# Kernel optimization log

Hardware: AMD Instinct MI355X
Metric: run time of the kernel (lower is better)

Reference implementation:

```python
import jax, jax.numpy as jnp
import numpy as np
from jax import lax

R = 3
D = (2 * R + 1) ** 2  # 49 local offsets


def _unfold(x, r):
    # torch F.unfold(kernel=2r+1, padding=r): (B,C,H,W) -> (B, C*K*K, H, W),
    # channel-major (c, ky, kx) ordering, matching conv_general_dilated_patches.
    k = 2 * r + 1
    return lax.conv_general_dilated_patches(
        x, (k, k), (1, 1), [(r, r), (r, r)],
        dimension_numbers=("NCHW", "OIHW", "NCHW"))


def _l2norm(x, eps=1e-12):
    n = jnp.sqrt(jnp.sum(x * x, axis=1, keepdims=True))
    return x / jnp.maximum(n, eps)


def setup_inputs() -> dict:
    key = jax.random.key(0)
    ks = jax.random.split(key, 8)
    B, Cin, Cmid, H, W = 2, 256, 128, 112, 112
    phi_cur = jax.random.normal(ks[0], (B, Cin, H, W), jnp.float32)
    phi_rnd = jax.random.normal(ks[1], (B, Cin, H, W), jnp.float32)
    P_cur = jax.random.normal(ks[2], (B, 3, H, W), jnp.float32)
    P_rnd = jax.random.normal(ks[3], (B, 3, H, W), jnp.float32)
    Wq = jax.random.normal(ks[4], (Cmid, Cin), jnp.float32) * 0.05
    Wk = jax.random.normal(ks[5], (Cmid, Cin), jnp.float32) * 0.05
    Wv = jax.random.normal(ks[6], (D, D), jnp.float32) * 0.1
    bv = jnp.zeros((D,), jnp.float32)
    gamma = jnp.array(1.0, jnp.float32)
    return dict(phi_cur=phi_cur, phi_rnd=phi_rnd, P_cur=P_cur, P_rnd=P_rnd,
                Wq=Wq, Wk=Wk, Wv=Wv, bv=bv, gamma=gamma)


def reference(phi_cur, phi_rnd, P_cur, P_rnd, Wq, Wk, Wv, bv, gamma):
    B, _, H, W = phi_cur.shape
    # 1x1 convs + channel L2 normalize
    q = _l2norm(jnp.einsum('oc,bchw->bohw', Wq, phi_cur))
    k = _l2norm(jnp.einsum('oc,bchw->bohw', Wk, phi_rnd))
    # local cost volume: patches (B, Cmid, D, H, W)
    patches = _unfold(k, R).reshape(B, -1, D, H, W)
    corr = jnp.einsum('bchw,bcdhw->bdhw', q, patches)  # (B,D,H,W)
    vol_corr = jnp.einsum('ed,bdhw->behw', Wv, corr) + bv[None, :, None, None]
    # geometric bias
    Pr = _unfold(P_rnd, R).reshape(B, 3, D, H, W)
    dP = P_cur[:, :, None, :, :] - Pr  # (B,3,D,H,W)
    dz = dP[:, 2]
    dist = jnp.sqrt(jnp.clip(jnp.sum(dP * dP, axis=1), 1e-12, None))
    logits = vol_corr + gamma * (-dist - 0.5 * jnp.abs(dz))
    w = jax.nn.softmax(logits, axis=1)
    off = jnp.arange(-R, R + 1, dtype=w.dtype)
    dY, dX = jnp.meshgrid(off, off, indexing='ij')
    offx = dX.reshape(1, D, 1, 1)
    offy = dY.reshape(1, D, 1, 1)
    du = jnp.sum(w * offx, axis=1, keepdims=True)
    dv = jnp.sum(w * offy, axis=1, keepdims=True)
    conf = jnp.max(w, axis=1, keepdims=True)
    return du, dv, conf
```

## Files before the change

### kernel.cpp

```cpp
#include <hip/hip_runtime.h>
#include <hip/hip_bf16.h>
#include <math.h>

constexpr int B    = 2;
constexpr int CIN  = 256;
constexpr int CMID = 128;
constexpr int H    = 112;
constexpr int W    = 112;
constexpr int HW   = H * W;
constexpr int NPIX = B * HW;
constexpr int RAD  = 3;
constexpr int KS   = 7;
constexpr int DD   = 49;

typedef __attribute__((ext_vector_type(8))) short  short8;
typedef __attribute__((ext_vector_type(4))) float  float4v;

__device__ __forceinline__ unsigned pkbf(float a, float b) {
    __hip_bfloat162 h = __float22bfloat162_rn(make_float2(a, b));
    union { __hip_bfloat162 h2; unsigned u; } c;
    c.h2 = h;
    return c.u;
}

constexpr int PSTR = 264;

__global__ __launch_bounds__(256) void proj_mfma(
    const float* __restrict__ phi_cur, const float* __restrict__ phi_rnd,
    const float* __restrict__ Wq, const float* __restrict__ Wk,
    unsigned short* __restrict__ q_ws, unsigned short* __restrict__ k_ws)
{
    __shared__ unsigned short pt[64 * PSTR];
    __shared__ float red[4][64];

    const int tid  = threadIdx.x;
    const int lane = tid & 63;
    const int wv   = __builtin_amdgcn_readfirstlane(tid >> 6);
    const int t    = blockIdx.y;

    const float* __restrict__ phi  = t ? phi_rnd : phi_cur;
    const float* __restrict__ Wf   = t ? Wk : Wq;
    unsigned short* __restrict__ outp = t ? k_ws : q_ws;

    const int pgb = blockIdx.x * 64;
    const int b   = pgb / HW;
    const int pim = pgb % HW;
    const float* pbase = phi + (size_t)b * CIN * HW + pim;

#pragma unroll
    for (int pass = 0; pass < 8; ++pass) {
        const int idx = pass * 256 + tid;
        const int cp  = idx >> 4;
        const int pq  = idx & 15;
        const int c0  = cp * 2;
        const float4 va = *(const float4*)(pbase + (size_t)c0 * HW + pq * 4);
        const float4 vb = *(const float4*)(pbase + (size_t)(c0 + 1) * HW + pq * 4);
        *(unsigned*)(pt + (pq * 4 + 0) * PSTR + c0) = pkbf(va.x, vb.x);
        *(unsigned*)(pt + (pq * 4 + 1) * PSTR + c0) = pkbf(va.y, vb.y);
        *(unsigned*)(pt + (pq * 4 + 2) * PSTR + c0) = pkbf(va.z, vb.z);
        *(unsigned*)(pt + (pq * 4 + 3) * PSTR + c0) = pkbf(va.w, vb.w);
    }

    const int m = lane & 15, quad = lane >> 4;
    short8 af[2][8];
#pragma unroll
    for (int ot = 0; ot < 2; ++ot)
#pragma unroll
        for (int kc = 0; kc < 8; ++kc) {
            const float* wr = Wf + (size_t)(wv * 32 + ot * 16 + m) * CIN
                                 + kc * 32 + quad * 8;
            const float4 w0 = *(const float4*)(wr);
            const float4 w1 = *(const float4*)(wr + 4);
            union { short8 s; unsigned u[4]; } cv;
            cv.u[0] = pkbf(w0.x, w0.y);
            cv.u[1] = pkbf(w0.z, w0.w);
            cv.u[2] = pkbf(w1.x, w1.y);
            cv.u[3] = pkbf(w1.z, w1.w);
            af[ot][kc] = cv.s;
        }

    __syncthreads();

    float4v acc[2][4];
#pragma unroll
    for (int ot = 0; ot < 2; ++ot)
#pragma unroll
        for (int nt = 0; nt < 4; ++nt) acc[ot][nt] = (float4v)0.f;

#pragma unroll
    for (int kc = 0; kc < 8; ++kc) {
        short8 bf[4];
#pragma unroll
        for (int nt = 0; nt < 4; ++nt)
            bf[nt] = *(const short8*)(pt + (nt * 16 + m) * PSTR + kc * 32 + quad * 8);
#pragma unroll
        for (int ot = 0; ot < 2; ++ot)
#pragma unroll
            for (int nt = 0; nt < 4; ++nt)
                acc[ot][nt] = __builtin_amdgcn_mfma_f32_16x16x32_bf16(
                    af[ot][kc], bf[nt], acc[ot][nt], 0, 0, 0);
    }

#pragma unroll
    for (int nt = 0; nt < 4; ++nt) {
        float ss = 0.f;
#pragma unroll
        for (int ot = 0; ot < 2; ++ot)
#pragma unroll
            for (int r = 0; r < 4; ++r)
                ss = fmaf(acc[ot][nt][r], acc[ot][nt][r], ss);
        ss += __shfl_xor(ss, 16, 64);
        ss += __shfl_xor(ss, 32, 64);
        if (quad == 0) red[wv][nt * 16 + m] = ss;
    }
    __syncthreads();

    float inv[4];
#pragma unroll
    for (int nt = 0; nt < 4; ++nt) {
        const int px = nt * 16 + m;
        const float tot = red[0][px] + red[1][px] + red[2][px] + red[3][px];
        inv[nt] = 1.f / fmaxf(sqrtf(tot), 1e-12f);
    }

#pragma unroll
    for (int nt = 0; nt < 4; ++nt)
#pragma unroll
        for (int ot = 0; ot < 2; ++ot) {
            uint2 st;
            st.x = pkbf(acc[ot][nt][0] * inv[nt], acc[ot][nt][1] * inv[nt]);
            st.y = pkbf(acc[ot][nt][2] * inv[nt], acc[ot][nt][3] * inv[nt]);
            *(uint2*)(outp + (size_t)(pgb + nt * 16 + m) * CMID
                      + wv * 32 + ot * 16 + quad * 4) = st;
        }
}

constexpr int TILE = 16;
constexpr int COLS = TILE + 6;
constexpr int NV   = KS * COLS;
constexpr int KSTR = 136;

__global__ __launch_bounds__(256) void corr_kernel(
    const unsigned short* __restrict__ q_ws, const unsigned short* __restrict__ k_ws,
    const float* __restrict__ P_cur, const float* __restrict__ P_rnd,
    const float* __restrict__ Wvm, const float* __restrict__ bv,
    const float* __restrict__ gamma_p, float* __restrict__ out)
{
    __shared__ unsigned short kt[NV * KSTR];
    __shared__ alignas(16) unsigned short qt[TILE * KSTR];
    __shared__ float cs[TILE][52];

    const int tid  = threadIdx.x;
    const int lane = tid & 63;
    const int wv   = __builtin_amdgcn_readfirstlane(tid >> 6);
    const int w0   = blockIdx.x * TILE;
    const int h    = blockIdx.y;
    const int b    = blockIdx.z;

    const int sub  = tid & 15;
    const int vgrp = tid >> 4;
#pragma unroll
    for (int pass = 0; pass < 10; ++pass) {
        const int vi = pass * 16 + vgrp;
        if (vi < NV) {
            const int rr = vi / COLS;
            const int cc = vi % COLS;
            const int hh = h + rr - RAD;
            const int ww = w0 + cc - RAD;
            uint4 v = make_uint4(0, 0, 0, 0);
            if (hh >= 0 && hh < H && ww >= 0 && ww < W)
                v = *(const uint4*)(k_ws + (size_t)(b * HW + hh * W + ww) * CMID + sub * 8);
            *(uint4*)(kt + vi * KSTR + sub * 8) = v;
        }
    }
    {
        const uint4 v = *(const uint4*)(q_ws + (size_t)(b * HW + h * W + w0 + vgrp) * CMID + sub * 8);
        *(uint4*)(qt + vgrp * KSTR + sub * 8) = v;
    }

    const int  ld    = (lane < DD) ? lane : 0;
    const bool valid = (lane < DD);
    float wrow[52];
#pragma unroll
    for (int e = 0; e < DD; ++e) wrow[e] = Wvm[ld * DD + e];
    wrow[49] = wrow[50] = wrow[51] = 0.f;
    const float bvv   = bv[ld];
    const float gamma = gamma_p[0];

    __syncthreads();

    if (tid < TILE * 3)
        cs[tid / 3][49 + tid % 3] = 0.f;

    const int m = lane & 15, quad = lane >> 4;
    for (int g = wv; g < 14; g += 4) {
        const int r  = g >> 1;
        const int nt = g & 1;
        const int vi = min(r * COLS + nt * 16 + m, NV - 1);
        float4v acc = (float4v)0.f;
#pragma unroll
        for (int kc = 0; kc < 4; ++kc) {
            const short8 afrag = *(const short8*)(qt + m * KSTR + kc * 32 + quad * 8);
            const short8 bfrag = *(const short8*)(kt + vi * KSTR + kc * 32 + quad * 8);
            acc = __builtin_amdgcn_mfma_f32_16x16x32_bf16(afrag, bfrag, acc, 0, 0, 0);
        }
#pragma unroll
        for (int reg = 0; reg < 4; ++reg) {
            const int p   = quad * 4 + reg;
            const int off = nt * 16 + m - p;
            if (off >= 0 && off <= 6)
                cs[p][r * 7 + off] = acc[reg];
        }
    }
    __syncthreads();
    float* lsf = reinterpret_cast<float*>(qt);

    const int dy = ld / KS - RAD;
    const int dx = ld % KS - RAD;

#pragma unroll
    for (int i = 0; i < 4; ++i) {
        const int pl = wv * 4 + i;

        const int hn = h + dy, wn = w0 + pl + dx;
        const bool inb = valid && hn >= 0 && hn < H && wn >= 0 && wn < W;
        const float* pc = P_cur + (size_t)b * 3 * HW + (h * W + w0 + pl);
        const float cx = pc[0], cy = pc[HW], cz = pc[2 * HW];
        float rx = 0.f, ry = 0.f, rz = 0.f;
        if (inb) {
            const float* pr = P_rnd + (size_t)b * 3 * HW + (hn * W + wn);
            rx = pr[0]; ry = pr[HW]; rz = pr[2 * HW];
        }
        const float dpx = cx - rx, dpy = cy - ry, dpz = cz - rz;
        const float dist = sqrtf(fmaxf(dpx * dpx + dpy * dpy + dpz * dpz, 1e-12f));

        float logit = -INFINITY;
        if (valid) {
            float v = bvv;
#pragma unroll
            for (int e4 = 0; e4 < 13; ++e4) {
                const float4 c4 = *(const float4*)&cs[pl][e4 * 4];
                v = fmaf(wrow[e4 * 4 + 0], c4.x, v);
                v = fmaf(wrow[e4 * 4 + 1], c4.y, v);
                v = fmaf(wrow[e4 * 4 + 2], c4.z, v);
                v = fmaf(wrow[e4 * 4 + 3], c4.w, v);
            }
            logit = v + gamma * (-dist - 0.5f * fabsf(dpz));
        }
        lsf[pl * 64 + lane] = logit;
    }

    {
        const int pli = lane >> 4;
        const int dq  = lane & 15;
        const int pl  = wv * 4 + pli;

        const float4 v = ((const float4*)lsf)[pl * 16 + dq];

        float m4 = fmaxf(fmaxf(v.x, v.y), fmaxf(v.z, v.w));
#pragma unroll
        for (int s = 1; s < 16; s <<= 1)
            m4 = fmaxf(m4, __shfl_xor(m4, s, 64));

        const float e0 = __expf(v.x - m4);
        const float e1 = __expf(v.y - m4);
        const float e2 = __expf(v.z - m4);
        const float e3 = __expf(v.w - m4);
        float Z = (e0 + e1) + (e2 + e3);

        const int c0i = dq * 4;
        float dus = 0.f, dvs = 0.f;
        {
            const float ex[4] = { e0, e1, e2, e3 };
#pragma unroll
            for (int j = 0; j < 4; ++j) {
                const int col = c0i + j;
                dus = fmaf(ex[j], (float)(col % KS - RAD), dus);
                dvs = fmaf(ex[j], (float)(col / KS - RAD), dvs);
            }
        }
#pragma unroll
        for (int s = 1; s < 16; s <<= 1) {
            Z   += __shfl_xor(Z,   s, 64);
            dus += __shfl_xor(dus, s, 64);
            dvs += __shfl_xor(dvs, s, 64);
        }

        if (dq == 0) {
            const int pg = b * HW + h * W + w0 + pl;
            const float invZ = 1.f / Z;
            out[pg]            = dus * invZ;
            out[NPIX + pg]     = dvs * invZ;
            out[2 * NPIX + pg] = invZ;
        }
    }
}

extern "C" void kernel_launch(void* const* d_in, const int* in_sizes, int n_in,
                              void* d_out, int out_size, void* d_ws, size_t ws_size,
                              hipStream_t stream)
{
    const float* phi_cur = (const float*)d_in[0];
    const float* phi_rnd = (const float*)d_in[1];
    const float* P_cur   = (const float*)d_in[2];
    const float* P_rnd   = (const float*)d_in[3];
    const float* Wq      = (const float*)d_in[4];
    const float* Wk      = (const float*)d_in[5];
    const float* Wv      = (const float*)d_in[6];
    const float* bv      = (const float*)d_in[7];
    const float* gm      = (const float*)d_in[8];
    float* out = (float*)d_out;

    unsigned short* ws   = (unsigned short*)d_ws;
    unsigned short* q_ws = ws;
    unsigned short* k_ws = q_ws + (size_t)NPIX * CMID;

    proj_mfma<<<dim3(NPIX / 64, 2), 256, 0, stream>>>(
        phi_cur, phi_rnd, Wq, Wk, q_ws, k_ws);

    corr_kernel<<<dim3(W / TILE, H, B), 256, 0, stream>>>(
        q_ws, k_ws, P_cur, P_rnd, Wv, bv, gm, out);
}
```

Baseline: 141.5 us.

## Pre-convert weights to bf16, swizzle LDS, remap corr blocks, split FMA chains

A new prep kernel converts Wq/Wk to bf16 once and pads Wv rows to 52 floats. The projection kernel then streams A fragments straight from the bf16 weights inside the k-loop instead of holding 16 short8 registers per thread. It also XOR-swizzles the LDS layout of the phi tile to cut bank conflicts, and its launch bounds now ask for 4 blocks per CU. The corr kernel remaps block IDs so neighbouring blocks are spread across XCDs, loads Wv as float4, and splits the 49-term dot product into two accumulators for more ILP. In exchange it adds an extra kernel launch and re-reads weights from global/L2 on every k step.

```diff
diff --git a/kernel.cpp b/kernel.cpp
--- a/kernel.cpp
+++ b/kernel.cpp
@@ -23,11 +23,34 @@
     return c.u;
 }
 
+__global__ __launch_bounds__(256) void prep(
+    const float* __restrict__ Wq, const float* __restrict__ Wk,
+    const float* __restrict__ Wv,
+    unsigned short* __restrict__ wqb, unsigned short* __restrict__ wkb,
+    float* __restrict__ wvp)
+{
+    if (blockIdx.x < 64) {
+        const int i  = blockIdx.x * 256 + threadIdx.x;
+        const int n4 = (CMID * CIN) / 4;
+        const float4 v = (i < n4) ? ((const float4*)Wq)[i] : ((const float4*)Wk)[i - n4];
+        uint2 r;
+        r.x = pkbf(v.x, v.y);
+        r.y = pkbf(v.z, v.w);
+        if (i < n4) ((uint2*)wqb)[i] = r;
+        else        ((uint2*)wkb)[i - n4] = r;
+    } else {
+        for (int idx = threadIdx.x; idx < DD * 52; idx += 256) {
+            const int r = idx / 52, c = idx % 52;
+            wvp[idx] = (c < DD) ? Wv[r * DD + c] : 0.f;
+        }
+    }
+}
+
 constexpr int PSTR = 264;
 
-__global__ __launch_bounds__(256) void proj_mfma(
+__global__ __launch_bounds__(256, 4) void proj_mfma(
     const float* __restrict__ phi_cur, const float* __restrict__ phi_rnd,
-    const float* __restrict__ Wq, const float* __restrict__ Wk,
+    const unsigned short* __restrict__ wq_bf, const unsigned short* __restrict__ wk_bf,
     unsigned short* __restrict__ q_ws, unsigned short* __restrict__ k_ws)
 {
     __shared__ unsigned short pt[64 * PSTR];
@@ -38,9 +61,9 @@
     const int wv   = __builtin_amdgcn_readfirstlane(tid >> 6);
     const int t    = blockIdx.y;
 
-    const float* __restrict__ phi  = t ? phi_rnd : phi_cur;
-    const float* __restrict__ Wf   = t ? Wk : Wq;
-    unsigned short* __restrict__ outp = t ? k_ws : q_ws;
+    const float* __restrict__ phi          = t ? phi_rnd : phi_cur;
+    const unsigned short* __restrict__ Wbf = t ? wk_bf : wq_bf;
+    unsigned short* __restrict__ outp      = t ? k_ws : q_ws;
 
     const int pgb = blockIdx.x * 64;
     const int b   = pgb / HW;
@@ -53,52 +76,43 @@
         const int cp  = idx >> 4;
         const int pq  = idx & 15;
         const int c0  = cp * 2;
+        const int swz = ((pq >> 1) & 3) << 3;
         const float4 va = *(const float4*)(pbase + (size_t)c0 * HW + pq * 4);
         const float4 vb = *(const float4*)(pbase + (size_t)(c0 + 1) * HW + pq * 4);
-        *(unsigned*)(pt + (pq * 4 + 0) * PSTR + c0) = pkbf(va.x, vb.x);
-        *(unsigned*)(pt + (pq * 4 + 1) * PSTR + c0) = pkbf(va.y, vb.y);
-        *(unsigned*)(pt + (pq * 4 + 2) * PSTR + c0) = pkbf(va.z, vb.z);
-        *(unsigned*)(pt + (pq * 4 + 3) * PSTR + c0) = pkbf(va.w, vb.w);
-    }
+        const int col = c0 ^ swz;
+        *(unsigned*)(pt + (pq * 4 + 0) * PSTR + col) = pkbf(va.x, vb.x);
+        *(unsigned*)(pt + (pq * 4 + 1) * PSTR + col) = pkbf(va.y, vb.y);
+        *(unsigned*)(pt + (pq * 4 + 2) * PSTR + col) = pkbf(va.z, vb.z);
+        *(unsigned*)(pt + (pq * 4 + 3) * PSTR + col) = pkbf(va.w, vb.w);
+    }
+
+    __syncthreads();
 
     const int m = lane & 15, quad = lane >> 4;
-    short8 af[2][8];
+    float4v acc[2][4];
 #pragma unroll
     for (int ot = 0; ot < 2; ++ot)
 #pragma unroll
-        for (int kc = 0; kc < 8; ++kc) {
-            const float* wr = Wf + (size_t)(wv * 32 + ot * 16 + m) * CIN
-                                 + kc * 32 + quad * 8;
-            const float4 w0 = *(const float4*)(wr);
-            const float4 w1 = *(const float4*)(wr + 4);
-            union { short8 s; unsigned u[4]; } cv;
-            cv.u[0] = pkbf(w0.x, w0.y);
-            cv.u[1] = pkbf(w0.z, w0.w);
-            cv.u[2] = pkbf(w1.x, w1.y);
-            cv.u[3] = pkbf(w1.z, w1.w);
-            af[ot][kc] = cv.s;
-        }
-
-    __syncthreads();
-
-    float4v acc[2][4];
-#pragma unroll
-    for (int ot = 0; ot < 2; ++ot)
-#pragma unroll
         for (int nt = 0; nt < 4; ++nt) acc[ot][nt] = (float4v)0.f;
 
 #pragma unroll
     for (int kc = 0; kc < 8; ++kc) {
-        short8 bf[4];
-#pragma unroll
-        for (int nt = 0; nt < 4; ++nt)
-            bf[nt] = *(const short8*)(pt + (nt * 16 + m) * PSTR + kc * 32 + quad * 8);
-#pragma unroll
-        for (int ot = 0; ot < 2; ++ot)
-#pragma unroll
-            for (int nt = 0; nt < 4; ++nt)
-                acc[ot][nt] = __builtin_amdgcn_mfma_f32_16x16x32_bf16(
-                    af[ot][kc], bf[nt], acc[ot][nt], 0, 0, 0);
+        const short8 af0 = *(const short8*)(Wbf +
+            (size_t)(wv * 32 + m) * CIN + kc * 32 + quad * 8);
+        const short8 af1 = *(const short8*)(Wbf +
+            (size_t)(wv * 32 + 16 + m) * CIN + kc * 32 + quad * 8);
+        short8 bfr[4];
+#pragma unroll
+        for (int nt = 0; nt < 4; ++nt) {
+            const int row = nt * 16 + m;
+            const int col = (kc * 32 + quad * 8) ^ (((row >> 3) & 3) << 3);
+            bfr[nt] = *(const short8*)(pt + row * PSTR + col);
+        }
+#pragma unroll
+        for (int nt = 0; nt < 4; ++nt) {
+            acc[0][nt] = __builtin_amdgcn_mfma_f32_16x16x32_bf16(af0, bfr[nt], acc[0][nt], 0, 0, 0);
+            acc[1][nt] = __builtin_amdgcn_mfma_f32_16x16x32_bf16(af1, bfr[nt], acc[1][nt], 0, 0, 0);
+        }
     }
 
 #pragma unroll
@@ -143,7 +157,7 @@
 __global__ __launch_bounds__(256) void corr_kernel(
     const unsigned short* __restrict__ q_ws, const unsigned short* __restrict__ k_ws,
     const float* __restrict__ P_cur, const float* __restrict__ P_rnd,
-    const float* __restrict__ Wvm, const float* __restrict__ bv,
+    const float* __restrict__ wvp, const float* __restrict__ bv,
     const float* __restrict__ gamma_p, float* __restrict__ out)
 {
     __shared__ unsigned short kt[NV * KSTR];
@@ -153,9 +167,13 @@
     const int tid  = threadIdx.x;
     const int lane = tid & 63;
     const int wv   = __builtin_amdgcn_readfirstlane(tid >> 6);
-    const int w0   = blockIdx.x * TILE;
-    const int h    = blockIdx.y;
-    const int b    = blockIdx.z;
+
+    const int fid = (blockIdx.z * H + blockIdx.y) * (W / TILE) + blockIdx.x;
+    const int swz = (fid & 7) * 196 + (fid >> 3);
+    const int b   = swz / (H * (W / TILE));
+    const int rem = swz % (H * (W / TILE));
+    const int h   = rem / (W / TILE);
+    const int w0  = (rem % (W / TILE)) * TILE;
 
     const int sub  = tid & 15;
     const int vgrp = tid >> 4;
@@ -180,10 +198,10 @@
 
     const int  ld    = (lane < DD) ? lane : 0;
     const bool valid = (lane < DD);
-    float wrow[52];
-#pragma unroll
-    for (int e = 0; e < DD; ++e) wrow[e] = Wvm[ld * DD + e];
-    wrow[49] = wrow[50] = wrow[51] = 0.f;
+    float4 wq4[13];
+#pragma unroll
+    for (int j = 0; j < 13; ++j)
+        wq4[j] = *(const float4*)(wvp + ld * 52 + j * 4);
     const float bvv   = bv[ld];
     const float gamma = gamma_p[0];
 
@@ -236,16 +254,24 @@
 
         float logit = -INFINITY;
         if (valid) {
-            float v = bvv;
+            float va0 = bvv, va1 = 0.f;
 #pragma unroll
             for (int e4 = 0; e4 < 13; ++e4) {
                 const float4 c4 = *(const float4*)&cs[pl][e4 * 4];
-                v = fmaf(wrow[e4 * 4 + 0], c4.x, v);
-                v = fmaf(wrow[e4 * 4 + 1], c4.y, v);
-                v = fmaf(wrow[e4 * 4 + 2], c4.z, v);
-                v = fmaf(wrow[e4 * 4 + 3], c4.w, v);
+                const float4 w4 = wq4[e4];
+                if (e4 & 1) {
+                    va1 = fmaf(w4.x, c4.x, va1);
+                    va1 = fmaf(w4.y, c4.y, va1);
+                    va1 = fmaf(w4.z, c4.z, va1);
+                    va1 = fmaf(w4.w, c4.w, va1);
+                } else {
+                    va0 = fmaf(w4.x, c4.x, va0);
+                    va0 = fmaf(w4.y, c4.y, va0);
+                    va0 = fmaf(w4.z, c4.z, va0);
+                    va0 = fmaf(w4.w, c4.w, va0);
+                }
             }
-            logit = v + gamma * (-dist - 0.5f * fabsf(dpz));
+            logit = (va0 + va1) + gamma * (-dist - 0.5f * fabsf(dpz));
         }
         lsf[pl * 64 + lane] = logit;
     }
@@ -314,10 +340,15 @@
     unsigned short* ws   = (unsigned short*)d_ws;
     unsigned short* q_ws = ws;
     unsigned short* k_ws = q_ws + (size_t)NPIX * CMID;
+    unsigned short* wqb  = k_ws + (size_t)NPIX * CMID;
+    unsigned short* wkb  = wqb + (size_t)CMID * CIN;
+    float*          wvp  = (float*)(wkb + (size_t)CMID * CIN);
+
+    prep<<<dim3(65), 256, 0, stream>>>(Wq, Wk, Wv, wqb, wkb, wvp);
 
     proj_mfma<<<dim3(NPIX / 64, 2), 256, 0, stream>>>(
-        phi_cur, phi_rnd, Wq, Wk, q_ws, k_ws);
+        phi_cur, phi_rnd, wqb, wkb, q_ws, k_ws);
 
     corr_kernel<<<dim3(W / TILE, H, B), 256, 0, stream>>>(
-        q_ws, k_ws, P_cur, P_rnd, Wv, bv, gm, out);
-}
+        q_ws, k_ws, P_cur, P_rnd, wvp, bv, gm, out);
+}
```

Result: faster. 138.4 us (-2.2%).
